# Kernel optimization log

Measured on AMD Instinct MI355X. Metric: run time of the kernel, lower is better.

Reference implementation:

```python
import jax, jax.numpy as jnp
import numpy as np


def _silu(x):
    return x * jax.nn.sigmoid(x)


def setup_inputs() -> dict:
    key = jax.random.key(0)
    ks = jax.random.split(key, 8)
    B, S, H, E, I, IS = 2, 1024, 2048, 64, 512, 1024
    s = 0.02  # weight init scale to keep activations in a sane range
    return {
        "hidden_states": jax.random.normal(ks[0], (B, S, H), jnp.float32),
        "gate_weight": jax.random.normal(ks[1], (E, H), jnp.float32) * s,   # router [E,H]
        "w_gate": jax.random.normal(ks[2], (E, H, I), jnp.float32) * s,
        "w_up": jax.random.normal(ks[3], (E, H, I), jnp.float32) * s,
        "w_down": jax.random.normal(ks[4], (E, I, H), jnp.float32) * s,
        "sw_gate": jax.random.normal(ks[5], (H, IS), jnp.float32) * s,
        "sw_up": jax.random.normal(ks[6], (H, IS), jnp.float32) * s,
        "sw_down": jax.random.normal(ks[7], (IS, H), jnp.float32) * s,
        "top_k": 6,
    }


def reference(hidden_states, gate_weight, w_gate, w_up, w_down,
              sw_gate, sw_up, sw_down, top_k):
    orig_shape = hidden_states.shape
    H = orig_shape[-1]
    x = hidden_states.reshape(-1, H)          # [T,H]
    T = x.shape[0]
    E = gate_weight.shape[0]

    # fp32 router (need_fp32_gate)
    logits = x.astype(jnp.float32) @ gate_weight.astype(jnp.float32).T   # [T,E]
    # sigmoid_routing_function: sigmoid -> normalize -> topk -> renormalize
    p = jax.nn.sigmoid(logits)
    p = p / jnp.sum(p, axis=-1, keepdims=True)
    topk_w, topk_idx = jax.lax.top_k(p, top_k)                           # [T,k]
    topk_w = topk_w / jnp.sum(topk_w, axis=-1, keepdims=True)            # renormalize

    # dense combine weights [T,E]: zero for unselected experts
    cw = jnp.zeros((T, E), x.dtype).at[jnp.arange(T)[:, None], topk_idx].set(
        topk_w.astype(x.dtype))

    # grouped SwiGLU expert FFN, combine weighted outputs; scan over experts
    # keeps peak memory at one [T,I] intermediate per step.
    def step(acc, ew):
        wg, wu, wd, c = ew                                               # c: [T]
        y = (_silu(x @ wg) * (x @ wu)) @ wd                              # [T,H]
        return acc + c[:, None] * y, None

    routed, _ = jax.lax.scan(step, jnp.zeros_like(x),
                             (w_gate, w_up, w_down, cw.T))

    # shared experts FFN over all tokens (returned separately, not reduced)
    shared_out = (_silu(x @ sw_gate) * (x @ sw_up)) @ sw_down            # [T,H]

    return shared_out, routed.reshape(orig_shape)
```

## Files before the change

### kernel.cpp

```cpp
#include <hip/hip_runtime.h>
#include <hip/hip_bf16.h>
#include <stdint.h>


#define H_DIM 2048
#define E_NUM 64
#define I_DIM 512
#define IS_DIM 1024
#define CAPR 288
#define TOPK_MAX 8
#define BK 64
#define LDP 68

typedef float f32x4 __attribute__((ext_vector_type(4)));
typedef __bf16 bf16x8 __attribute__((ext_vector_type(8)));

__device__ __forceinline__ uint16_t f2bf(float f) {
  union { float f; uint32_t u; } v;
  v.f = f;
  uint32_t r = (v.u + 0x7FFFu + ((v.u >> 16) & 1u)) >> 16;
  return (uint16_t)r;
}
__device__ __forceinline__ uint32_t pack2(float a, float b) {
  return (uint32_t)f2bf(a) | ((uint32_t)f2bf(b) << 16);
}
__device__ __forceinline__ float bf2f(uint16_t b) {
  union { uint32_t u; float f; } v;
  v.u = (uint32_t)b << 16;
  return v.f;
}

#define BAR()                                              \
  do {                                                     \
    asm volatile("s_waitcnt lgkmcnt(0)" ::: "memory");     \
    __builtin_amdgcn_s_barrier();                          \
    asm volatile("" ::: "memory");                         \
  } while (0)

__global__ __launch_bounds__(256) void router_kernel(
    const float* __restrict__ x, const float* __restrict__ gw,
    const int* __restrict__ topk_ptr, int* __restrict__ cnt,
    int* __restrict__ bucket, float* __restrict__ bw,
    uint16_t* __restrict__ xbK, const int T) {
  const int t = blockIdx.x;
  const int tid = threadIdx.x;
  __shared__ float xs[H_DIM];
  __shared__ float logits[E_NUM];
#pragma unroll
  for (int i = 0; i < 2; ++i) {
    int idx = tid + i * 256;
    *(float4*)(&xs[idx * 4]) = *(const float4*)(x + (size_t)t * H_DIM + idx * 4);
  }
  __syncthreads();
  {
    const float* p = &xs[tid * 8];
    uint4 o;
    o.x = pack2(p[0], p[1]);
    o.y = pack2(p[2], p[3]);
    o.z = pack2(p[4], p[5]);
    o.w = pack2(p[6], p[7]);
    *(uint4*)(xbK + (size_t)(tid >> 2) * T * 32 + (size_t)t * 32 +
              (tid & 3) * 8) = o;
  }
  const int lane = tid & 63, wid = tid >> 6;
  float xr[32];
#pragma unroll
  for (int it = 0; it < 32; ++it) xr[it] = xs[lane + 64 * it];
  for (int eo = 0; eo < 16; ++eo) {
    int e = wid + eo * 4;
    const float* g = gw + (size_t)e * H_DIM;
    float acc = 0.f;
#pragma unroll
    for (int it = 0; it < 32; ++it) acc += xr[it] * g[lane + 64 * it];
#pragma unroll
    for (int off = 32; off; off >>= 1) acc += __shfl_xor(acc, off);
    if (lane == 0) logits[e] = acc;
  }
  __syncthreads();
  if (wid == 0) {
    int k = topk_ptr[0];
    if (k > TOPK_MAX) k = TOPK_MAX;
    float v = 1.f / (1.f + expf(-logits[lane]));
    float s = 0.f, myw = 0.f;
    int mye = 0;
    for (int j = 0; j < k; ++j) {
      float m = v;
      int mi = lane;
#pragma unroll
      for (int off = 32; off; off >>= 1) {
        float ov = __shfl_xor(m, off);
        int oi = __shfl_xor(mi, off);
        if (ov > m || (ov == m && oi < mi)) { m = ov; mi = oi; }
      }
      if (lane == j) { myw = m; mye = mi; }
      if (lane == mi) v = -1e30f;
      s += m;
    }
    if (lane < k) {
      float w = myw / s;
      int pos = atomicAdd(&cnt[mye], 1);
      if (pos < CAPR) {
        bucket[mye * CAPR + pos] = t * 8 + lane;
        bw[mye * CAPR + pos] = w;
      }
    }
  }
}

__global__ __launch_bounds__(256) void gather_xe(
    const uint16_t* __restrict__ xbK, const int* __restrict__ cnt,
    const int* __restrict__ bucket, uint16_t* __restrict__ xe, const int T) {
  const int e = blockIdx.x;
  const int kgrp = blockIdx.y & 15, sgrp = blockIdx.y >> 4;
  const int tid = threadIdx.x;
  const int slot = sgrp * 64 + (tid & 63);
  const int kblk = kgrp * 4 + (tid >> 6);
  const int n_e = min(cnt[e], CAPR);
  if (slot >= n_e) return;
  const int t = bucket[e * CAPR + slot] >> 3;
  const uint4* src = (const uint4*)(xbK + (size_t)kblk * T * 32 + (size_t)t * 32);
  uint4* dst = (uint4*)(xe + (size_t)e * (64 * CAPR * 32) +
                        (size_t)kblk * (CAPR * 32) + (size_t)slot * 32);
#pragma unroll
  for (int j = 0; j < 4; ++j) dst[j] = src[j];
}

template <int BM, bool GATHER>
__device__ __forceinline__ void ffn_in_body(
    uint16_t (*Bgs)[32][LDP], uint16_t (*Bus)[32][LDP],
    const uint16_t* __restrict__ A0, const float* __restrict__ Wg,
    const float* __restrict__ Wu, uint16_t* __restrict__ actO,
    const int* __restrict__ cnt, const int K, const int ldb, const int SLOTS,
    const int bid) {
  constexpr int MF = BM / 64;
  constexpr int NF = 2;

  int e = 0, nt, mt0, mtE, n_e;
  const float *Bg, *Bu;
  const uint16_t* AE;
  uint16_t* outE;
  if constexpr (GATHER) {
    e = bid & 63;
    nt = bid >> 6;
    n_e = min(cnt[e], CAPR);
    mt0 = 0;
    mtE = (n_e + BM - 1) / BM;
    const size_t wo = (size_t)e * K * ldb;
    Bg = Wg + wo;
    Bu = Wu + wo;
    AE = A0 + (size_t)e * (64 * CAPR * 32);
    outE = actO + (size_t)e * ((I_DIM / 32) * CAPR * 32);
  } else {
    nt = bid & 31;
    mt0 = bid >> 5;
    mtE = mt0 + 1;
    n_e = 1 << 30;
    Bg = Wg;
    Bu = Wu;
    AE = A0;
    outE = actO;
  }
  if (mt0 * BM >= n_e) return;

  const int tid = threadIdx.x;
  const int cg4 = (tid & 7) * 4, kp = tid >> 3;
  const float* bgp = Bg + (size_t)(2 * kp) * ldb + nt * 32 + cg4;
  const float* bup = Bu + (size_t)(2 * kp) * ldb + nt * 32 + cg4;

  const int lane = tid & 63, wid = tid >> 6;
  const int fr = lane & 15, kg = lane >> 4;
  const int wrow = wid * (BM / 4);
  const size_t ldA = (size_t)SLOTS * 32;

  float4 g0, g1, u0, u1;
  const int NS = K / BK;

  for (int mt = mt0; mt < mtE; ++mt) {
    const uint16_t* ab[MF];
#pragma unroll
    for (int mf = 0; mf < MF; ++mf)
      ab[mf] = AE + (size_t)(mt * BM + wrow + mf * 16 + fr) * 32 + kg * 8;

    f32x4 accg[MF][NF] = {};
    f32x4 accu[MF][NF] = {};

    g0 = *(const float4*)bgp;
    g1 = *(const float4*)(bgp + ldb);
    u0 = *(const float4*)bup;
    u1 = *(const float4*)(bup + ldb);
    {
      const int k2 = 2 * kp;
      *(uint32_t*)(&Bgs[0][cg4 + 0][k2]) = pack2(g0.x, g1.x);
      *(uint32_t*)(&Bgs[0][cg4 + 1][k2]) = pack2(g0.y, g1.y);
      *(uint32_t*)(&Bgs[0][cg4 + 2][k2]) = pack2(g0.z, g1.z);
      *(uint32_t*)(&Bgs[0][cg4 + 3][k2]) = pack2(g0.w, g1.w);
      *(uint32_t*)(&Bus[0][cg4 + 0][k2]) = pack2(u0.x, u1.x);
      *(uint32_t*)(&Bus[0][cg4 + 1][k2]) = pack2(u0.y, u1.y);
      *(uint32_t*)(&Bus[0][cg4 + 2][k2]) = pack2(u0.z, u1.z);
      *(uint32_t*)(&Bus[0][cg4 + 3][k2]) = pack2(u0.w, u1.w);
    }
    if (NS > 1) {
      const float* g = bgp + (size_t)BK * ldb;
      g0 = *(const float4*)g;
      g1 = *(const float4*)(g + ldb);
      const float* u = bup + (size_t)BK * ldb;
      u0 = *(const float4*)u;
      u1 = *(const float4*)(u + ldb);
    }
    BAR();

    int b = 0;
    for (int s = 0; s < NS; ++s) {
      uint4 a[MF][2];
#pragma unroll
      for (int mf = 0; mf < MF; ++mf)
#pragma unroll
        for (int sl = 0; sl < 2; ++sl)
          a[mf][sl] = *(const uint4*)(ab[mf] + (size_t)(2 * s + sl) * ldA);
      if (s + 1 < NS) {
        const int k2 = 2 * kp;
        *(uint32_t*)(&Bgs[b ^ 1][cg4 + 0][k2]) = pack2(g0.x, g1.x);
        *(uint32_t*)(&Bgs[b ^ 1][cg4 + 1][k2]) = pack2(g0.y, g1.y);
        *(uint32_t*)(&Bgs[b ^ 1][cg4 + 2][k2]) = pack2(g0.z, g1.z);
        *(uint32_t*)(&Bgs[b ^ 1][cg4 + 3][k2]) = pack2(g0.w, g1.w);
        *(uint32_t*)(&Bus[b ^ 1][cg4 + 0][k2]) = pack2(u0.x, u1.x);
        *(uint32_t*)(&Bus[b ^ 1][cg4 + 1][k2]) = pack2(u0.y, u1.y);
        *(uint32_t*)(&Bus[b ^ 1][cg4 + 2][k2]) = pack2(u0.z, u1.z);
        *(uint32_t*)(&Bus[b ^ 1][cg4 + 3][k2]) = pack2(u0.w, u1.w);
      }
      if (s + 2 < NS) {
        const float* g = bgp + (size_t)((s + 2) * BK) * ldb;
        g0 = *(const float4*)g;
        g1 = *(const float4*)(g + ldb);
        const float* u = bup + (size_t)((s + 2) * BK) * ldb;
        u0 = *(const float4*)u;
        u1 = *(const float4*)(u + ldb);
      }
#pragma unroll
      for (int sl = 0; sl < 2; ++sl)
#pragma unroll
        for (int nf = 0; nf < NF; ++nf) {
          const bf16x8 bg = __builtin_bit_cast(
              bf16x8, *(const uint4*)(&Bgs[b][nf * 16 + fr][kg * 8 + sl * 32]));
          const bf16x8 bu = __builtin_bit_cast(
              bf16x8, *(const uint4*)(&Bus[b][nf * 16 + fr][kg * 8 + sl * 32]));
#pragma unroll
          for (int mf = 0; mf < MF; ++mf) {
            const bf16x8 af = __builtin_bit_cast(bf16x8, a[mf][sl]);
            accg[mf][nf] = __builtin_amdgcn_mfma_f32_16x16x32_bf16(
                af, bg, accg[mf][nf], 0, 0, 0);
            accu[mf][nf] = __builtin_amdgcn_mfma_f32_16x16x32_bf16(
                af, bu, accu[mf][nf], 0, 0, 0);
          }
        }
      BAR();
      b ^= 1;
    }

#pragma unroll
    for (int mf = 0; mf < MF; ++mf)
#pragma unroll
      for (int rr = 0; rr < 4; ++rr) {
        const int slot = mt * BM + wrow + mf * 16 + kg * 4 + rr;
        if (slot < n_e) {
          uint16_t* op = outE + (size_t)nt * ldA + (size_t)slot * 32 + fr;
#pragma unroll
          for (int nf = 0; nf < NF; ++nf) {
            const float g = accg[mf][nf][rr], u = accu[mf][nf][rr];
            op[nf * 16] = f2bf(g / (1.f + expf(-g)) * u);
          }
        }
      }
  }
}

__global__ __launch_bounds__(256) void fused_in(
    const uint16_t* __restrict__ xe, const float* __restrict__ Wg,
    const float* __restrict__ Wu, uint16_t* __restrict__ act,
    const int* __restrict__ cnt,
    const uint16_t* __restrict__ xbK, const float* __restrict__ sWg,
    const float* __restrict__ sWu, uint16_t* __restrict__ s_actK, const int T) {
  __shared__ uint16_t Bgs[2][32][LDP];
  __shared__ uint16_t Bus[2][32][LDP];
  const int bx = blockIdx.x;
  if (bx < E_NUM * (I_DIM / 32)) {
    ffn_in_body<256, true>(Bgs, Bus, xe, Wg, Wu, act, cnt, H_DIM, I_DIM, CAPR,
                           bx);
  } else {
    ffn_in_body<128, false>(Bgs, Bus, xbK, sWg, sWu, s_actK, nullptr, H_DIM,
                            IS_DIM, T, bx - E_NUM * (I_DIM / 32));
  }
}

template <int BM, bool GATHER>
__device__ __forceinline__ void ffn_down_body(
    uint16_t (*Bs)[64][LDP], const uint16_t* __restrict__ A0,
    const float* __restrict__ Wd, void* __restrict__ outp,
    const int* __restrict__ cnt, const int* __restrict__ bucket,
    const float* __restrict__ bw, const int K, const int SLOTS, const int bid) {
  constexpr int MF = BM / 64;
  constexpr int NF = 4;

  int e = 0, nt, mt0, mtE, n_e;
  const float* Bd;
  const uint16_t* AE;
  if constexpr (GATHER) {
    e = bid & 63;
    nt = bid >> 6;
    n_e = min(cnt[e], CAPR);
    mt0 = 0;
    mtE = (n_e + BM - 1) / BM;
    AE = A0 + (size_t)e * ((I_DIM / 32) * CAPR * 32);
    Bd = Wd + (size_t)e * K * H_DIM;
  } else {
    nt = bid & 31;
    mt0 = bid >> 5;
    mtE = mt0 + 1;
    n_e = 1 << 30;
    AE = A0;
    Bd = Wd;
  }
  if (mt0 * BM >= n_e) return;

  const int tid = threadIdx.x;
  const int cg4 = (tid & 15) * 4, kp = tid >> 4;
  const float* bdp = Bd + (size_t)(2 * kp) * H_DIM + nt * 64 + cg4;

  const int lane = tid & 63, wid = tid >> 6;
  const int fr = lane & 15, kg = lane >> 4;
  const int wrow = wid * (BM / 4);
  const size_t ldA = (size_t)SLOTS * 32;

  float4 d0[2], d1[2];
  const int NS = K / BK;

  for (int mt = mt0; mt < mtE; ++mt) {
    const uint16_t* ab[MF];
#pragma unroll
    for (int mf = 0; mf < MF; ++mf)
      ab[mf] = AE + (size_t)(mt * BM + wrow + mf * 16 + fr) * 32 + kg * 8;

    f32x4 acc[MF][NF] = {};

#pragma unroll
    for (int pp = 0; pp < 2; ++pp) {
      const float* d = bdp + (size_t)(2 * pp * 16) * H_DIM;
      d0[pp] = *(const float4*)d;
      d1[pp] = *(const float4*)(d + H_DIM);
    }
#pragma unroll
    for (int pp = 0; pp < 2; ++pp) {
      const int k2 = 2 * (kp + pp * 16);
      *(uint32_t*)(&Bs[0][cg4 + 0][k2]) = pack2(d0[pp].x, d1[pp].x);
      *(uint32_t*)(&Bs[0][cg4 + 1][k2]) = pack2(d0[pp].y, d1[pp].y);
      *(uint32_t*)(&Bs[0][cg4 + 2][k2]) = pack2(d0[pp].z, d1[pp].z);
      *(uint32_t*)(&Bs[0][cg4 + 3][k2]) = pack2(d0[pp].w, d1[pp].w);
    }
    if (NS > 1) {
#pragma unroll
      for (int pp = 0; pp < 2; ++pp) {
        const float* d = bdp + (size_t)(BK + 2 * pp * 16) * H_DIM;
        d0[pp] = *(const float4*)d;
        d1[pp] = *(const float4*)(d + H_DIM);
      }
    }
    BAR();

    int b = 0;
    for (int s = 0; s < NS; ++s) {
      uint4 a[MF][2];
#pragma unroll
      for (int mf = 0; mf < MF; ++mf)
#pragma unroll
        for (int sl = 0; sl < 2; ++sl)
          a[mf][sl] = *(const uint4*)(ab[mf] + (size_t)(2 * s + sl) * ldA);
      if (s + 1 < NS) {
#pragma unroll
        for (int pp = 0; pp < 2; ++pp) {
          const int k2 = 2 * (kp + pp * 16);
          *(uint32_t*)(&Bs[b ^ 1][cg4 + 0][k2]) = pack2(d0[pp].x, d1[pp].x);
          *(uint32_t*)(&Bs[b ^ 1][cg4 + 1][k2]) = pack2(d0[pp].y, d1[pp].y);
          *(uint32_t*)(&Bs[b ^ 1][cg4 + 2][k2]) = pack2(d0[pp].z, d1[pp].z);
          *(uint32_t*)(&Bs[b ^ 1][cg4 + 3][k2]) = pack2(d0[pp].w, d1[pp].w);
        }
      }
      if (s + 2 < NS) {
#pragma unroll
        for (int pp = 0; pp < 2; ++pp) {
          const float* d = bdp + (size_t)((s + 2) * BK + 2 * pp * 16) * H_DIM;
          d0[pp] = *(const float4*)d;
          d1[pp] = *(const float4*)(d + H_DIM);
        }
      }
#pragma unroll
      for (int sl = 0; sl < 2; ++sl)
#pragma unroll
        for (int nf = 0; nf < NF; ++nf) {
          const bf16x8 bf_ = __builtin_bit_cast(
              bf16x8, *(const uint4*)(&Bs[b][nf * 16 + fr][kg * 8 + sl * 32]));
#pragma unroll
          for (int mf = 0; mf < MF; ++mf) {
            const bf16x8 af = __builtin_bit_cast(bf16x8, a[mf][sl]);
            acc[mf][nf] = __builtin_amdgcn_mfma_f32_16x16x32_bf16(
                af, bf_, acc[mf][nf], 0, 0, 0);
          }
        }
      BAR();
      b ^= 1;
    }

    const int col0 = nt * 64 + fr;
#pragma unroll
    for (int mf = 0; mf < MF; ++mf)
#pragma unroll
      for (int rr = 0; rr < 4; ++rr) {
        const int slot = mt * BM + wrow + mf * 16 + kg * 4 + rr;
        if constexpr (GATHER) {
          if (slot < n_e) {
            const int bv = bucket[e * CAPR + slot];
            const float w = bw[e * CAPR + slot];
            uint16_t* yb = (uint16_t*)outp + (size_t)bv * H_DIM + col0;
#pragma unroll
            for (int nf = 0; nf < NF; ++nf)
              yb[nf * 16] = f2bf(w * acc[mf][nf][rr]);
          }
        } else {
          float* op = (float*)outp + (size_t)slot * H_DIM + col0;
#pragma unroll
          for (int nf = 0; nf < NF; ++nf) op[nf * 16] = acc[mf][nf][rr];
        }
      }
  }
}

__global__ __launch_bounds__(256) void moe_down_k(
    const uint16_t* __restrict__ act, const float* __restrict__ Wd,
    uint16_t* __restrict__ ybuf, const int* __restrict__ cnt,
    const int* __restrict__ bucket, const float* __restrict__ bw) {
  __shared__ uint16_t Bs[2][64][LDP];
  ffn_down_body<256, true>(Bs, act, Wd, (void*)ybuf, cnt, bucket, bw, I_DIM,
                           CAPR, blockIdx.x);
}
__global__ __launch_bounds__(256) void dense_down_k(
    const uint16_t* __restrict__ s_actK, const float* __restrict__ sWd,
    float* __restrict__ shared_out, const int T) {
  __shared__ uint16_t Bs[2][64][LDP];
  ffn_down_body<128, false>(Bs, s_actK, sWd, (void*)shared_out, nullptr,
                            nullptr, nullptr, IS_DIM, T, blockIdx.x);
}

__global__ __launch_bounds__(256) void combine_kernel(
    const uint16_t* __restrict__ ybuf, const int* __restrict__ topk_ptr,
    float* __restrict__ routed) {
  const int t = blockIdx.x;
  const int tid = threadIdx.x;
  int k = topk_ptr[0];
  if (k > TOPK_MAX) k = TOPK_MAX;
  float acc[8] = {};
  const uint16_t* base = ybuf + (size_t)t * 8 * H_DIM + tid * 8;
  for (int j = 0; j < k; ++j) {
    uint4 v = *(const uint4*)(base + (size_t)j * H_DIM);
    const uint16_t* h = (const uint16_t*)&v;
#pragma unroll
    for (int i = 0; i < 8; ++i) acc[i] += bf2f(h[i]);
  }
  float* op = routed + (size_t)t * H_DIM + tid * 8;
  *(float4*)op = make_float4(acc[0], acc[1], acc[2], acc[3]);
  *(float4*)(op + 4) = make_float4(acc[4], acc[5], acc[6], acc[7]);
}

extern "C" void kernel_launch(void* const* d_in, const int* in_sizes, int n_in,
                              void* d_out, int out_size, void* d_ws, size_t ws_size,
                              hipStream_t stream) {
  const float* x = (const float*)d_in[0];
  const float* gw = (const float*)d_in[1];
  const float* w_gate = (const float*)d_in[2];
  const float* w_up = (const float*)d_in[3];
  const float* w_down = (const float*)d_in[4];
  const float* sw_gate = (const float*)d_in[5];
  const float* sw_up = (const float*)d_in[6];
  const float* sw_down = (const float*)d_in[7];
  const int* topk = (const int*)d_in[8];
  const int T = in_sizes[0] / H_DIM;

  float* shared_out = (float*)d_out;
  float* routed = shared_out + (size_t)T * H_DIM;

  char* ws = (char*)d_ws;
  size_t off = 0;
  auto take = [&](size_t b) {
    char* p = ws + off;
    off += (b + 255) & ~(size_t)255;
    return p;
  };
  uint16_t* xbK = (uint16_t*)take((size_t)T * H_DIM * 2);
  int* cnt = (int*)take(E_NUM * 4);
  int* bucket = (int*)take((size_t)E_NUM * CAPR * 4);
  float* bw = (float*)take((size_t)E_NUM * CAPR * 4);
  uint16_t* xe = (uint16_t*)take((size_t)E_NUM * 64 * CAPR * 32 * 2 + 65536);
  uint16_t* act = (uint16_t*)take((size_t)E_NUM * 16 * CAPR * 32 * 2 + 65536);
  uint16_t* s_actK = (uint16_t*)take((size_t)(IS_DIM / 32) * T * 32 * 2);
  uint16_t* ybuf = (uint16_t*)take((size_t)T * 8 * H_DIM * 2);

  hipMemsetAsync(cnt, 0, E_NUM * 4, stream);

  router_kernel<<<T, 256, 0, stream>>>(x, gw, topk, cnt, bucket, bw, xbK, T);
  gather_xe<<<dim3(E_NUM, 16 * ((CAPR + 63) / 64)), 256, 0, stream>>>(
      xbK, cnt, bucket, xe, T);

  fused_in<<<E_NUM * (I_DIM / 32) + (IS_DIM / 32) * (T / 128), 256, 0, stream>>>(
      xe, w_gate, w_up, act, cnt, xbK, sw_gate, sw_up, s_actK, T);
  moe_down_k<<<E_NUM * (H_DIM / 64), 256, 0, stream>>>(act, w_down, ybuf, cnt,
                                                       bucket, bw);
  dense_down_k<<<(H_DIM / 64) * (T / 128), 256, 0, stream>>>(s_actK, sw_down,
                                                             shared_out, T);
  combine_kernel<<<T, 256, 0, stream>>>(ybuf, topk, routed);
}
```

Baseline: 514.4 us.

## Gather expert tokens directly in GEMM, drop gather kernel, truncate bf16 packing

Removes the gather_xe kernel and its xe staging buffer. The expert gate/up GEMM now reads activation rows straight from the K-blocked bf16 input through bucket indices. The fused launch is split back into separate routed and shared kernels, and the down kernel clamps out-of-range slots to a valid index. Weight conversion now uses truncating bf16 packing via a byte-permute instead of round-to-nearest, which trims ALU work but changes rounding behaviour. The indexed loads are scattered rather than contiguous, and splitting the kernels loses the overlap the merged launch gave between routed and shared work.

```diff
diff --git a/kernel.cpp b/kernel.cpp
--- a/kernel.cpp
+++ b/kernel.cpp
@@ -23,6 +23,10 @@
 }
 __device__ __forceinline__ uint32_t pack2(float a, float b) {
   return (uint32_t)f2bf(a) | ((uint32_t)f2bf(b) << 16);
+}
+__device__ __forceinline__ uint32_t pk2t(float a, float b) {
+  return __builtin_amdgcn_perm(__builtin_bit_cast(uint32_t, b),
+                               __builtin_bit_cast(uint32_t, a), 0x07060302u);
 }
 __device__ __forceinline__ float bf2f(uint16_t b) {
   union { uint32_t u; float f; } v;
@@ -107,38 +111,20 @@
   }
 }
 
-__global__ __launch_bounds__(256) void gather_xe(
-    const uint16_t* __restrict__ xbK, const int* __restrict__ cnt,
-    const int* __restrict__ bucket, uint16_t* __restrict__ xe, const int T) {
-  const int e = blockIdx.x;
-  const int kgrp = blockIdx.y & 15, sgrp = blockIdx.y >> 4;
-  const int tid = threadIdx.x;
-  const int slot = sgrp * 64 + (tid & 63);
-  const int kblk = kgrp * 4 + (tid >> 6);
-  const int n_e = min(cnt[e], CAPR);
-  if (slot >= n_e) return;
-  const int t = bucket[e * CAPR + slot] >> 3;
-  const uint4* src = (const uint4*)(xbK + (size_t)kblk * T * 32 + (size_t)t * 32);
-  uint4* dst = (uint4*)(xe + (size_t)e * (64 * CAPR * 32) +
-                        (size_t)kblk * (CAPR * 32) + (size_t)slot * 32);
-#pragma unroll
-  for (int j = 0; j < 4; ++j) dst[j] = src[j];
-}
-
 template <int BM, bool GATHER>
 __device__ __forceinline__ void ffn_in_body(
     uint16_t (*Bgs)[32][LDP], uint16_t (*Bus)[32][LDP],
     const uint16_t* __restrict__ A0, const float* __restrict__ Wg,
     const float* __restrict__ Wu, uint16_t* __restrict__ actO,
-    const int* __restrict__ cnt, const int K, const int ldb, const int SLOTS,
-    const int bid) {
+    const int* __restrict__ cnt, const int* __restrict__ bucket,
+    const int K, const int ldb, const int T, const int bid) {
   constexpr int MF = BM / 64;
   constexpr int NF = 2;
 
   int e = 0, nt, mt0, mtE, n_e;
   const float *Bg, *Bu;
-  const uint16_t* AE;
   uint16_t* outE;
+  size_t ldOut;
   if constexpr (GATHER) {
     e = bid & 63;
     nt = bid >> 6;
@@ -148,8 +134,8 @@
     const size_t wo = (size_t)e * K * ldb;
     Bg = Wg + wo;
     Bu = Wu + wo;
-    AE = A0 + (size_t)e * (64 * CAPR * 32);
     outE = actO + (size_t)e * ((I_DIM / 32) * CAPR * 32);
+    ldOut = (size_t)CAPR * 32;
   } else {
     nt = bid & 31;
     mt0 = bid >> 5;
@@ -157,8 +143,8 @@
     n_e = 1 << 30;
     Bg = Wg;
     Bu = Wu;
-    AE = A0;
     outE = actO;
+    ldOut = (size_t)T * 32;
   }
   if (mt0 * BM >= n_e) return;
 
@@ -170,7 +156,7 @@
   const int lane = tid & 63, wid = tid >> 6;
   const int fr = lane & 15, kg = lane >> 4;
   const int wrow = wid * (BM / 4);
-  const size_t ldA = (size_t)SLOTS * 32;
+  const size_t ldA = (size_t)T * 32;
 
   float4 g0, g1, u0, u1;
   const int NS = K / BK;
@@ -178,8 +164,16 @@
   for (int mt = mt0; mt < mtE; ++mt) {
     const uint16_t* ab[MF];
 #pragma unroll
-    for (int mf = 0; mf < MF; ++mf)
-      ab[mf] = AE + (size_t)(mt * BM + wrow + mf * 16 + fr) * 32 + kg * 8;
+    for (int mf = 0; mf < MF; ++mf) {
+      const int slot = mt * BM + wrow + mf * 16 + fr;
+      if constexpr (GATHER) {
+        const int idx = slot < n_e ? slot : 0;
+        const int t = bucket[e * CAPR + idx] >> 3;
+        ab[mf] = A0 + (size_t)t * 32 + kg * 8;
+      } else {
+        ab[mf] = A0 + (size_t)slot * 32 + kg * 8;
+      }
+    }
 
     f32x4 accg[MF][NF] = {};
     f32x4 accu[MF][NF] = {};
@@ -190,14 +184,14 @@
     u1 = *(const float4*)(bup + ldb);
     {
       const int k2 = 2 * kp;
-      *(uint32_t*)(&Bgs[0][cg4 + 0][k2]) = pack2(g0.x, g1.x);
-      *(uint32_t*)(&Bgs[0][cg4 + 1][k2]) = pack2(g0.y, g1.y);
-      *(uint32_t*)(&Bgs[0][cg4 + 2][k2]) = pack2(g0.z, g1.z);
-      *(uint32_t*)(&Bgs[0][cg4 + 3][k2]) = pack2(g0.w, g1.w);
-      *(uint32_t*)(&Bus[0][cg4 + 0][k2]) = pack2(u0.x, u1.x);
-      *(uint32_t*)(&Bus[0][cg4 + 1][k2]) = pack2(u0.y, u1.y);
-      *(uint32_t*)(&Bus[0][cg4 + 2][k2]) = pack2(u0.z, u1.z);
-      *(uint32_t*)(&Bus[0][cg4 + 3][k2]) = pack2(u0.w, u1.w);
+      *(uint32_t*)(&Bgs[0][cg4 + 0][k2]) = pk2t(g0.x, g1.x);
+      *(uint32_t*)(&Bgs[0][cg4 + 1][k2]) = pk2t(g0.y, g1.y);
+      *(uint32_t*)(&Bgs[0][cg4 + 2][k2]) = pk2t(g0.z, g1.z);
+      *(uint32_t*)(&Bgs[0][cg4 + 3][k2]) = pk2t(g0.w, g1.w);
+      *(uint32_t*)(&Bus[0][cg4 + 0][k2]) = pk2t(u0.x, u1.x);
+      *(uint32_t*)(&Bus[0][cg4 + 1][k2]) = pk2t(u0.y, u1.y);
+      *(uint32_t*)(&Bus[0][cg4 + 2][k2]) = pk2t(u0.z, u1.z);
+      *(uint32_t*)(&Bus[0][cg4 + 3][k2]) = pk2t(u0.w, u1.w);
     }
     if (NS > 1) {
       const float* g = bgp + (size_t)BK * ldb;
@@ -219,14 +213,14 @@
           a[mf][sl] = *(const uint4*)(ab[mf] + (size_t)(2 * s + sl) * ldA);
       if (s + 1 < NS) {
         const int k2 = 2 * kp;
-        *(uint32_t*)(&Bgs[b ^ 1][cg4 + 0][k2]) = pack2(g0.x, g1.x);
-        *(uint32_t*)(&Bgs[b ^ 1][cg4 + 1][k2]) = pack2(g0.y, g1.y);
-        *(uint32_t*)(&Bgs[b ^ 1][cg4 + 2][k2]) = pack2(g0.z, g1.z);
-        *(uint32_t*)(&Bgs[b ^ 1][cg4 + 3][k2]) = pack2(g0.w, g1.w);
-        *(uint32_t*)(&Bus[b ^ 1][cg4 + 0][k2]) = pack2(u0.x, u1.x);
-        *(uint32_t*)(&Bus[b ^ 1][cg4 + 1][k2]) = pack2(u0.y, u1.y);
-        *(uint32_t*)(&Bus[b ^ 1][cg4 + 2][k2]) = pack2(u0.z, u1.z);
-        *(uint32_t*)(&Bus[b ^ 1][cg4 + 3][k2]) = pack2(u0.w, u1.w);
+        *(uint32_t*)(&Bgs[b ^ 1][cg4 + 0][k2]) = pk2t(g0.x, g1.x);
+        *(uint32_t*)(&Bgs[b ^ 1][cg4 + 1][k2]) = pk2t(g0.y, g1.y);
+        *(uint32_t*)(&Bgs[b ^ 1][cg4 + 2][k2]) = pk2t(g0.z, g1.z);
+        *(uint32_t*)(&Bgs[b ^ 1][cg4 + 3][k2]) = pk2t(g0.w, g1.w);
+        *(uint32_t*)(&Bus[b ^ 1][cg4 + 0][k2]) = pk2t(u0.x, u1.x);
+        *(uint32_t*)(&Bus[b ^ 1][cg4 + 1][k2]) = pk2t(u0.y, u1.y);
+        *(uint32_t*)(&Bus[b ^ 1][cg4 + 2][k2]) = pk2t(u0.z, u1.z);
+        *(uint32_t*)(&Bus[b ^ 1][cg4 + 3][k2]) = pk2t(u0.w, u1.w);
       }
       if (s + 2 < NS) {
         const float* g = bgp + (size_t)((s + 2) * BK) * ldb;
@@ -263,7 +257,7 @@
       for (int rr = 0; rr < 4; ++rr) {
         const int slot = mt * BM + wrow + mf * 16 + kg * 4 + rr;
         if (slot < n_e) {
-          uint16_t* op = outE + (size_t)nt * ldA + (size_t)slot * 32 + fr;
+          uint16_t* op = outE + (size_t)nt * ldOut + (size_t)slot * 32 + fr;
 #pragma unroll
           for (int nf = 0; nf < NF; ++nf) {
             const float g = accg[mf][nf][rr], u = accu[mf][nf][rr];
@@ -274,22 +268,22 @@
   }
 }
 
-__global__ __launch_bounds__(256) void fused_in(
-    const uint16_t* __restrict__ xe, const float* __restrict__ Wg,
+__global__ __launch_bounds__(256) void moe_in_k(
+    const uint16_t* __restrict__ xbK, const float* __restrict__ Wg,
     const float* __restrict__ Wu, uint16_t* __restrict__ act,
-    const int* __restrict__ cnt,
+    const int* __restrict__ cnt, const int* __restrict__ bucket, const int T) {
+  __shared__ uint16_t Bgs[2][32][LDP];
+  __shared__ uint16_t Bus[2][32][LDP];
+  ffn_in_body<256, true>(Bgs, Bus, xbK, Wg, Wu, act, cnt, bucket, H_DIM, I_DIM,
+                         T, blockIdx.x);
+}
+__global__ __launch_bounds__(256) void dense_in_k(
     const uint16_t* __restrict__ xbK, const float* __restrict__ sWg,
     const float* __restrict__ sWu, uint16_t* __restrict__ s_actK, const int T) {
   __shared__ uint16_t Bgs[2][32][LDP];
   __shared__ uint16_t Bus[2][32][LDP];
-  const int bx = blockIdx.x;
-  if (bx < E_NUM * (I_DIM / 32)) {
-    ffn_in_body<256, true>(Bgs, Bus, xe, Wg, Wu, act, cnt, H_DIM, I_DIM, CAPR,
-                           bx);
-  } else {
-    ffn_in_body<128, false>(Bgs, Bus, xbK, sWg, sWu, s_actK, nullptr, H_DIM,
-                            IS_DIM, T, bx - E_NUM * (I_DIM / 32));
-  }
+  ffn_in_body<128, false>(Bgs, Bus, xbK, sWg, sWu, s_actK, nullptr, nullptr,
+                          H_DIM, IS_DIM, T, blockIdx.x);
 }
 
 template <int BM, bool GATHER>
@@ -337,8 +331,11 @@
   for (int mt = mt0; mt < mtE; ++mt) {
     const uint16_t* ab[MF];
 #pragma unroll
-    for (int mf = 0; mf < MF; ++mf)
-      ab[mf] = AE + (size_t)(mt * BM + wrow + mf * 16 + fr) * 32 + kg * 8;
+    for (int mf = 0; mf < MF; ++mf) {
+      const int slot = mt * BM + wrow + mf * 16 + fr;
+      const int idx = slot < n_e ? slot : 0;
+      ab[mf] = AE + (size_t)idx * 32 + kg * 8;
+    }
 
     f32x4 acc[MF][NF] = {};
 
@@ -351,10 +348,10 @@
 #pragma unroll
     for (int pp = 0; pp < 2; ++pp) {
       const int k2 = 2 * (kp + pp * 16);
-      *(uint32_t*)(&Bs[0][cg4 + 0][k2]) = pack2(d0[pp].x, d1[pp].x);
-      *(uint32_t*)(&Bs[0][cg4 + 1][k2]) = pack2(d0[pp].y, d1[pp].y);
-      *(uint32_t*)(&Bs[0][cg4 + 2][k2]) = pack2(d0[pp].z, d1[pp].z);
-      *(uint32_t*)(&Bs[0][cg4 + 3][k2]) = pack2(d0[pp].w, d1[pp].w);
+      *(uint32_t*)(&Bs[0][cg4 + 0][k2]) = pk2t(d0[pp].x, d1[pp].x);
+      *(uint32_t*)(&Bs[0][cg4 + 1][k2]) = pk2t(d0[pp].y, d1[pp].y);
+      *(uint32_t*)(&Bs[0][cg4 + 2][k2]) = pk2t(d0[pp].z, d1[pp].z);
+      *(uint32_t*)(&Bs[0][cg4 + 3][k2]) = pk2t(d0[pp].w, d1[pp].w);
     }
     if (NS > 1) {
 #pragma unroll
@@ -378,10 +375,10 @@
 #pragma unroll
         for (int pp = 0; pp < 2; ++pp) {
           const int k2 = 2 * (kp + pp * 16);
-          *(uint32_t*)(&Bs[b ^ 1][cg4 + 0][k2]) = pack2(d0[pp].x, d1[pp].x);
-          *(uint32_t*)(&Bs[b ^ 1][cg4 + 1][k2]) = pack2(d0[pp].y, d1[pp].y);
-          *(uint32_t*)(&Bs[b ^ 1][cg4 + 2][k2]) = pack2(d0[pp].z, d1[pp].z);
-          *(uint32_t*)(&Bs[b ^ 1][cg4 + 3][k2]) = pack2(d0[pp].w, d1[pp].w);
+          *(uint32_t*)(&Bs[b ^ 1][cg4 + 0][k2]) = pk2t(d0[pp].x, d1[pp].x);
+          *(uint32_t*)(&Bs[b ^ 1][cg4 + 1][k2]) = pk2t(d0[pp].y, d1[pp].y);
+          *(uint32_t*)(&Bs[b ^ 1][cg4 + 2][k2]) = pk2t(d0[pp].z, d1[pp].z);
+          *(uint32_t*)(&Bs[b ^ 1][cg4 + 3][k2]) = pk2t(d0[pp].w, d1[pp].w);
         }
       }
       if (s + 2 < NS) {
@@ -497,7 +494,6 @@
   int* cnt = (int*)take(E_NUM * 4);
   int* bucket = (int*)take((size_t)E_NUM * CAPR * 4);
   float* bw = (float*)take((size_t)E_NUM * CAPR * 4);
-  uint16_t* xe = (uint16_t*)take((size_t)E_NUM * 64 * CAPR * 32 * 2 + 65536);
   uint16_t* act = (uint16_t*)take((size_t)E_NUM * 16 * CAPR * 32 * 2 + 65536);
   uint16_t* s_actK = (uint16_t*)take((size_t)(IS_DIM / 32) * T * 32 * 2);
   uint16_t* ybuf = (uint16_t*)take((size_t)T * 8 * H_DIM * 2);
@@ -505,14 +501,14 @@
   hipMemsetAsync(cnt, 0, E_NUM * 4, stream);
 
   router_kernel<<<T, 256, 0, stream>>>(x, gw, topk, cnt, bucket, bw, xbK, T);
-  gather_xe<<<dim3(E_NUM, 16 * ((CAPR + 63) / 64)), 256, 0, stream>>>(
-      xbK, cnt, bucket, xe, T);
-
-  fused_in<<<E_NUM * (I_DIM / 32) + (IS_DIM / 32) * (T / 128), 256, 0, stream>>>(
-      xe, w_gate, w_up, act, cnt, xbK, sw_gate, sw_up, s_actK, T);
+
+  moe_in_k<<<E_NUM * (I_DIM / 32), 256, 0, stream>>>(xbK, w_gate, w_up, act,
+                                                     cnt, bucket, T);
   moe_down_k<<<E_NUM * (H_DIM / 64), 256, 0, stream>>>(act, w_down, ybuf, cnt,
                                                        bucket, bw);
+  combine_kernel<<<T, 256, 0, stream>>>(ybuf, topk, routed);
+  dense_in_k<<<(IS_DIM / 32) * (T / 128), 256, 0, stream>>>(xbK, sw_gate,
+                                                            sw_up, s_actK, T);
   dense_down_k<<<(H_DIM / 64) * (T / 128), 256, 0, stream>>>(s_actK, sw_down,
                                                              shared_out, T);
-  combine_kernel<<<T, 256, 0, stream>>>(ybuf, topk, routed);
-}
+}
```

Measured after the change: 471.4 us. 8.4% less time.
